# Performance work log

Measured on AMD Instinct MI355X. Metric: run time of the kernel, lower is better.

Reference implementation:

```python
import jax, jax.numpy as jnp
import numpy as np

NUM_HEADS = 16


def setup_inputs() -> dict:
    key = jax.random.key(0)
    ks = jax.random.split(key, 6)
    B, S, D = 2, 2048, 1024
    hidden_states = jax.random.normal(ks[0], (B, S, D), dtype=jnp.float32)
    attention_mask = jnp.zeros((B, 1, 1, S), dtype=jnp.float32)  # additive mask
    # Linear weights stored as [in, out] (equivalent to torch weight.T)
    W_qkv = jax.random.normal(ks[1], (D, 3 * D), dtype=jnp.float32) * (1.0 / np.sqrt(D))
    b_qkv = jnp.zeros((3 * D,), dtype=jnp.float32)
    W_proj = jax.random.normal(ks[2], (D, D), dtype=jnp.float32) * (1.0 / np.sqrt(D))
    b_proj = jnp.zeros((D,), dtype=jnp.float32)
    return {
        "hidden_states": hidden_states,
        "attention_mask": attention_mask,
        "W_qkv": W_qkv,
        "b_qkv": b_qkv,
        "W_proj": W_proj,
        "b_proj": b_proj,
    }


def reference(hidden_states, attention_mask, W_qkv, b_qkv, W_proj, b_proj):
    B, S, D = hidden_states.shape
    H = NUM_HEADS
    hd = D // H
    scale = 1.0 / jnp.sqrt(jnp.asarray(hd, hidden_states.dtype))

    qkv = hidden_states @ W_qkv + b_qkv            # [B,S,3D]
    q, k, v = jnp.split(qkv, 3, axis=-1)
    # [B,S,D] -> [B,H,S,hd]
    split_heads = lambda t: t.reshape(B, S, H, hd).transpose(0, 2, 1, 3)
    q, k, v = split_heads(q), split_heads(k), split_heads(v)

    scores = jnp.einsum("bhqd,bhkd->bhqk", q, k) * scale + attention_mask
    attn = jax.nn.softmax(scores, axis=-1)
    ctx = jnp.einsum("bhqk,bhkd->bhqd", attn, v)   # [B,H,S,hd]
    ctx = ctx.transpose(0, 2, 1, 3).reshape(B, S, D)
    return ctx @ W_proj + b_proj
```

## Files before the change

kernel.cpp:

```cpp
#include <hip/hip_runtime.h>
#include <hip/hip_bf16.h>

typedef short short8 __attribute__((ext_vector_type(8)));
typedef float floatx4 __attribute__((ext_vector_type(4)));

#define S_LEN 2048
#define DMODEL 1024
#define NH 16
#define HD 64
#define BATCH 2

static __device__ __forceinline__ short f2bf(float x) {
    __hip_bfloat16 h = __float2bfloat16(x);
    return *(short*)&h;
}

static __device__ __forceinline__ void async_ld16(const __hip_bfloat16* g, __hip_bfloat16* l) {
    __builtin_amdgcn_global_load_lds(
        (const __attribute__((address_space(1))) unsigned int*)g,
        (__attribute__((address_space(3))) unsigned int*)l, 16, 0, 0);
}

__global__ __launch_bounds__(256) void cvt_kernel(const float* __restrict__ X,
                                                  __hip_bfloat16* __restrict__ Y) {
    int i = (blockIdx.x * 256 + threadIdx.x) * 8;
    floatx4 f0 = *(const floatx4*)&X[i];
    floatx4 f1 = *(const floatx4*)&X[i + 4];
    short8 s;
    s[0] = f2bf(f0[0]); s[1] = f2bf(f0[1]); s[2] = f2bf(f0[2]); s[3] = f2bf(f0[3]);
    s[4] = f2bf(f1[0]); s[5] = f2bf(f1[1]); s[6] = f2bf(f1[2]); s[7] = f2bf(f1[3]);
    *(short8*)&Y[i] = s;
}

__global__ void transpose_kernel(const float* __restrict__ W,
                                 __hip_bfloat16* __restrict__ Wt, int K, int N) {
    __shared__ float tile[32][33];
    int n0 = blockIdx.x * 32, k0 = blockIdx.y * 32;
    int tx = threadIdx.x, ty = threadIdx.y;
#pragma unroll
    for (int i = 0; i < 32; i += 8)
        tile[ty + i][tx] = W[(size_t)(k0 + ty + i) * N + n0 + tx];
    __syncthreads();
#pragma unroll
    for (int i = 0; i < 32; i += 8)
        Wt[(size_t)(n0 + ty + i) * K + k0 + tx] = __float2bfloat16(tile[tx][ty + i]);
}

__global__ __launch_bounds__(256) void gemm128(
    const __hip_bfloat16* __restrict__ A, const __hip_bfloat16* __restrict__ Bt,
    const float* __restrict__ bias, float* __restrict__ Cf,
    __hip_bfloat16* __restrict__ Qp, __hip_bfloat16* __restrict__ Kp,
    __hip_bfloat16* __restrict__ Vt, int M, int N, int K, int mode) {
    __shared__ __align__(16) __hip_bfloat16 As[128 * 32];
    __shared__ __align__(16) __hip_bfloat16 Bs[128 * 32];
    const int m0 = blockIdx.y * 128, n0 = blockIdx.x * 128;
    const int t = threadIdx.x;
    const int wave = t >> 6, lane = t & 63;
    const int quad = lane >> 4, m16 = lane & 15;
    const int wm = (wave >> 1) * 64, wn = (wave & 1) * 64;
    const int srow = lane >> 2, scol = (lane & 3) * 8;

    floatx4 acc[4][4] = {};
    for (int k0 = 0; k0 < K; k0 += 32) {
#pragma unroll
        for (int i = 0; i < 2; i++) {
            const int rbase = wave * 32 + i * 16;
            async_ld16(&A[(size_t)(m0 + rbase + srow) * K + k0 + scol], &As[rbase * 32]);
            async_ld16(&Bt[(size_t)(n0 + rbase + srow) * K + k0 + scol], &Bs[rbase * 32]);
        }
        __syncthreads();
        short8 af[4], bfr[4];
#pragma unroll
        for (int i = 0; i < 4; i++)
            af[i] = *(const short8*)&As[(wm + i * 16 + m16) * 32 + quad * 8];
#pragma unroll
        for (int j = 0; j < 4; j++)
            bfr[j] = *(const short8*)&Bs[(wn + j * 16 + m16) * 32 + quad * 8];
#pragma unroll
        for (int i = 0; i < 4; i++)
#pragma unroll
            for (int j = 0; j < 4; j++)
                acc[i][j] = __builtin_amdgcn_mfma_f32_16x16x32_bf16(af[i], bfr[j], acc[i][j], 0, 0, 0);
        __syncthreads();
    }
#pragma unroll
    for (int i = 0; i < 4; i++)
#pragma unroll
        for (int j = 0; j < 4; j++) {
            int col = n0 + wn + j * 16 + m16;
            float bv = bias[col];
#pragma unroll
            for (int r = 0; r < 4; r++) {
                int row = m0 + wm + i * 16 + quad * 4 + r;
                float v = acc[i][j][r] + bv;
                if (mode == 0) {
                    Cf[(size_t)row * N + col] = v;
                } else {
                    __hip_bfloat16 hv = __float2bfloat16(v);
                    int tt = col >> 10, rem = col & 1023;
                    int h = rem >> 6, d = rem & 63;
                    int b = row >> 11, s = row & 2047;
                    if (tt == 0)      Qp[((size_t)(b * NH + h) * S_LEN + s) * HD + d] = hv;
                    else if (tt == 1) Kp[((size_t)(b * NH + h) * S_LEN + s) * HD + d] = hv;
                    else              Vt[((size_t)(b * NH + h) * HD + d) * S_LEN + s] = hv;
                }
            }
        }
}

__global__ __launch_bounds__(256) void attn_kernel(
    const __hip_bfloat16* __restrict__ Q,
    const __hip_bfloat16* __restrict__ K,
    const __hip_bfloat16* __restrict__ Vt,
    const float* __restrict__ mask,
    __hip_bfloat16* __restrict__ ctx) {
    __shared__ __align__(16) __hip_bfloat16 Ks[2][32 * 64];
    __shared__ __align__(16) __hip_bfloat16 Vs[2][64 * 32];
    __shared__ __align__(16) __hip_bfloat16 Ps[4][16][40];
    const int bh = blockIdx.x;
    const int b = bh >> 4, h = bh & 15;
    const int t = threadIdx.x, wave = t >> 6, lane = t & 63;
    const int quad = lane >> 4, m16 = lane & 15;
    const int qbase = blockIdx.y * 64 + wave * 16;
    const __hip_bfloat16* Qh = Q + (size_t)bh * S_LEN * HD;
    const __hip_bfloat16* Kh = K + (size_t)bh * S_LEN * HD;
    const __hip_bfloat16* Vh = Vt + (size_t)bh * HD * S_LEN;
    const float* mb = mask + (size_t)b * S_LEN;
    const float LOG2E = 1.44269504f;
    const float scale2 = 0.125f * LOG2E;
    const float M_FIX2 = 20.0f * LOG2E;

    const int kr = lane >> 3, kc = lane & 7;
    const size_t kgoff = (size_t)(wave * 8 + kr) * HD + ((kc ^ (kr & 7)) * 8);
    const int vr = lane >> 2, vc = lane & 3;
    const size_t vgoff = (size_t)(wave * 16 + vr) * S_LEN + ((vc ^ (vr & 3)) * 8);
    __hip_bfloat16* kdst0 = &Ks[0][wave * 512]; __hip_bfloat16* kdst1 = &Ks[1][wave * 512];
    __hip_bfloat16* vdst0 = &Vs[0][wave * 512]; __hip_bfloat16* vdst1 = &Vs[1][wave * 512];

    short8 aq0 = *(const short8*)&Qh[(size_t)(qbase + m16) * HD + quad * 8];
    short8 aq1 = *(const short8*)&Qh[(size_t)(qbase + m16) * HD + 32 + quad * 8];

    const short ONEB = (short)0x3F80;
    const short8 ones = {ONEB, ONEB, ONEB, ONEB, ONEB, ONEB, ONEB, ONEB};

    async_ld16(&Kh[kgoff], kdst0);
    async_ld16(&Vh[vgoff], vdst0);
    __syncthreads();

    floatx4 o[4] = {};
    floatx4 lacc = {};

    const int swk = m16 & 7;
    const int pc0 = (((m16 >> 3) ^ quad) << 3) | (m16 & 7);
    const int pc1 = ((((m16 >> 3) + 2) ^ quad) << 3) | (m16 & 7);
    const int apoff = (quad ^ ((m16 >> 2) & 3)) * 8;

    for (int it = 0; it < S_LEN / 32; it++) {
        const int k0 = it * 32;
        const int cur = it & 1;
        if (it < S_LEN / 32 - 1) {
            async_ld16(&Kh[(size_t)(k0 + 32) * HD + kgoff], cur ? kdst0 : kdst1);
            async_ld16(&Vh[(size_t)(k0 + 32) + vgoff], cur ? vdst0 : vdst1);
        }

        const __hip_bfloat16* Kc = Ks[cur];
        short8 bk00 = *(const short8*)&Kc[m16 * 64 + ((quad ^ swk) * 8)];
        short8 bk01 = *(const short8*)&Kc[m16 * 64 + (((quad + 4) ^ swk) * 8)];
        short8 bk10 = *(const short8*)&Kc[(16 + m16) * 64 + ((quad ^ swk) * 8)];
        short8 bk11 = *(const short8*)&Kc[(16 + m16) * 64 + (((quad + 4) ^ swk) * 8)];
        floatx4 sc0 = {}, sc1 = {};
        __builtin_amdgcn_s_setprio(1);
        sc0 = __builtin_amdgcn_mfma_f32_16x16x32_bf16(aq0, bk00, sc0, 0, 0, 0);
        sc0 = __builtin_amdgcn_mfma_f32_16x16x32_bf16(aq1, bk01, sc0, 0, 0, 0);
        sc1 = __builtin_amdgcn_mfma_f32_16x16x32_bf16(aq0, bk10, sc1, 0, 0, 0);
        sc1 = __builtin_amdgcn_mfma_f32_16x16x32_bf16(aq1, bk11, sc1, 0, 0, 0);
        __builtin_amdgcn_s_setprio(0);

        float mk0 = mb[k0 + m16] * LOG2E - M_FIX2;
        float mk1 = mb[k0 + 16 + m16] * LOG2E - M_FIX2;
#pragma unroll
        for (int r = 0; r < 4; r++) {
            float p0 = __builtin_amdgcn_exp2f(sc0[r] * scale2 + mk0);
            float p1 = __builtin_amdgcn_exp2f(sc1[r] * scale2 + mk1);
            Ps[wave][quad * 4 + r][pc0] = __float2bfloat16(p0);
            Ps[wave][quad * 4 + r][pc1] = __float2bfloat16(p1);
        }
        short8 ap = *(const short8*)&Ps[wave][m16][apoff];
        const __hip_bfloat16* Vc = Vs[cur];
        __builtin_amdgcn_s_setprio(1);
        lacc = __builtin_amdgcn_mfma_f32_16x16x32_bf16(ap, ones, lacc, 0, 0, 0);
#pragma unroll
        for (int tt = 0; tt < 4; tt++) {
            const int d = tt * 16 + m16;
            short8 bv = *(const short8*)&Vc[d * 32 + ((quad ^ (d & 3)) * 8)];
            o[tt] = __builtin_amdgcn_mfma_f32_16x16x32_bf16(ap, bv, o[tt], 0, 0, 0);
        }
        __builtin_amdgcn_s_setprio(0);
        __syncthreads();
    }

    float li[4];
#pragma unroll
    for (int r = 0; r < 4; r++) li[r] = 1.0f / lacc[r];
#pragma unroll
    for (int tt = 0; tt < 4; tt++)
#pragma unroll
        for (int r = 0; r < 4; r++) {
            int srow = qbase + quad * 4 + r;
            int d = tt * 16 + m16;
            float v = o[tt][r] * li[r];
            ctx[((size_t)b * S_LEN + srow) * DMODEL + h * HD + d] = __float2bfloat16(v);
        }
}

extern "C" void kernel_launch(void* const* d_in, const int* in_sizes, int n_in,
                              void* d_out, int out_size, void* d_ws, size_t ws_size,
                              hipStream_t stream) {
    (void)in_sizes; (void)n_in; (void)out_size; (void)ws_size;
    const float* hidden = (const float*)d_in[0];
    const float* mask   = (const float*)d_in[1];
    const float* Wqkv   = (const float*)d_in[2];
    const float* bqkv   = (const float*)d_in[3];
    const float* Wproj  = (const float*)d_in[4];
    const float* bproj  = (const float*)d_in[5];
    float* out = (float*)d_out;

    __hip_bfloat16* ws = (__hip_bfloat16*)d_ws;
    const size_t Q4 = 4u * 1024 * 1024;
    __hip_bfloat16* Qp      = ws;
    __hip_bfloat16* Kp      = ws + 1 * Q4;
    __hip_bfloat16* Vt      = ws + 2 * Q4;
    __hip_bfloat16* hid_bf  = ws + 3 * Q4;
    __hip_bfloat16* ctx     = ws + 3 * Q4;
    __hip_bfloat16* Wqkv_t  = ws + 4 * Q4;
    __hip_bfloat16* Wproj_t = ws + 4 * Q4;

    cvt_kernel<<<dim3(4 * 1024 * 1024 / 2048), 256, 0, stream>>>(hidden, hid_bf);
    transpose_kernel<<<dim3(3072 / 32, 1024 / 32), dim3(32, 8), 0, stream>>>(Wqkv, Wqkv_t, 1024, 3072);

    gemm128<<<dim3(3072 / 128, 4096 / 128), 256, 0, stream>>>(
        hid_bf, Wqkv_t, bqkv, nullptr, Qp, Kp, Vt, BATCH * S_LEN, 3 * DMODEL, DMODEL, 1);

    transpose_kernel<<<dim3(1024 / 32, 1024 / 32), dim3(32, 8), 0, stream>>>(Wproj, Wproj_t, 1024, 1024);

    attn_kernel<<<dim3(BATCH * NH, S_LEN / 64), 256, 0, stream>>>(Qp, Kp, Vt, mask, ctx);

    gemm128<<<dim3(1024 / 128, 4096 / 128), 256, 0, stream>>>(
        ctx, Wproj_t, bproj, out, nullptr, nullptr, nullptr, BATCH * S_LEN, DMODEL, DMODEL, 0);
}
```

Baseline: 228.5 us.

## Keep attention probabilities in registers via transposed QK^T and lane swizzle

The attention kernel now computes S^T (K as the A operand, Q as B), so each lane holds the probabilities it needs for the PV MFMA. A ds_swizzle exchange between lane pairs replaces the per-wave LDS round-trip through the Ps buffer. The key/value tile grows from 32 to 64 keys per iteration, which halves the loop trip count and barriers and doubles LDS for K/V, and launch_bounds now requests 4 blocks per CU. The lane mapping is intricate, so a permutation error would silently give wrong results, and the larger tiles raise register and LDS pressure.

```diff
diff --git a/kernel.cpp b/kernel.cpp
--- a/kernel.cpp
+++ b/kernel.cpp
@@ -3,6 +3,7 @@
 
 typedef short short8 __attribute__((ext_vector_type(8)));
 typedef float floatx4 __attribute__((ext_vector_type(4)));
+typedef int intx4 __attribute__((ext_vector_type(4)));
 
 #define S_LEN 2048
 #define DMODEL 1024
@@ -13,6 +14,12 @@
 static __device__ __forceinline__ short f2bf(float x) {
     __hip_bfloat16 h = __float2bfloat16(x);
     return *(short*)&h;
+}
+
+static __device__ __forceinline__ unsigned pk2(float lo, float hi) {
+    unsigned a = (unsigned)(unsigned short)f2bf(lo);
+    unsigned b = (unsigned)(unsigned short)f2bf(hi);
+    return a | (b << 16);
 }
 
 static __device__ __forceinline__ void async_ld16(const __hip_bfloat16* g, __hip_bfloat16* l) {
@@ -108,15 +115,14 @@
         }
 }
 
-__global__ __launch_bounds__(256) void attn_kernel(
+__global__ __launch_bounds__(256, 4) void attn_kernel(
     const __hip_bfloat16* __restrict__ Q,
     const __hip_bfloat16* __restrict__ K,
     const __hip_bfloat16* __restrict__ Vt,
     const float* __restrict__ mask,
     __hip_bfloat16* __restrict__ ctx) {
-    __shared__ __align__(16) __hip_bfloat16 Ks[2][32 * 64];
-    __shared__ __align__(16) __hip_bfloat16 Vs[2][64 * 32];
-    __shared__ __align__(16) __hip_bfloat16 Ps[4][16][40];
+    __shared__ __align__(16) __hip_bfloat16 Ks[2][64 * 64];
+    __shared__ __align__(16) __hip_bfloat16 Vs[2][64 * 64];
     const int bh = blockIdx.x;
     const int b = bh >> 4, h = bh & 15;
     const int t = threadIdx.x, wave = t >> 6, lane = t & 63;
@@ -130,12 +136,11 @@
     const float scale2 = 0.125f * LOG2E;
     const float M_FIX2 = 20.0f * LOG2E;
 
-    const int kr = lane >> 3, kc = lane & 7;
-    const size_t kgoff = (size_t)(wave * 8 + kr) * HD + ((kc ^ (kr & 7)) * 8);
-    const int vr = lane >> 2, vc = lane & 3;
-    const size_t vgoff = (size_t)(wave * 16 + vr) * S_LEN + ((vc ^ (vr & 3)) * 8);
-    __hip_bfloat16* kdst0 = &Ks[0][wave * 512]; __hip_bfloat16* kdst1 = &Ks[1][wave * 512];
-    __hip_bfloat16* vdst0 = &Vs[0][wave * 512]; __hip_bfloat16* vdst1 = &Vs[1][wave * 512];
+    const int r8 = lane >> 3, c8 = lane & 7;
+    const int kg0 = (wave * 16 + r8) * HD + ((c8 ^ r8) * 8);
+    const int kg1 = (wave * 16 + 8 + r8) * HD + ((c8 ^ r8) * 8);
+    const int vg0 = (wave * 16 + r8) * S_LEN + ((c8 ^ r8) * 8);
+    const int vg1 = (wave * 16 + 8 + r8) * S_LEN + ((c8 ^ r8) * 8);
 
     short8 aq0 = *(const short8*)&Qh[(size_t)(qbase + m16) * HD + quad * 8];
     short8 aq1 = *(const short8*)&Qh[(size_t)(qbase + m16) * HD + 32 + quad * 8];
@@ -143,57 +148,97 @@
     const short ONEB = (short)0x3F80;
     const short8 ones = {ONEB, ONEB, ONEB, ONEB, ONEB, ONEB, ONEB, ONEB};
 
-    async_ld16(&Kh[kgoff], kdst0);
-    async_ld16(&Vh[vgoff], vdst0);
+    {
+        __hip_bfloat16* kd = &Ks[0][wave * 16 * 64];
+        async_ld16(&Kh[kg0], kd);
+        async_ld16(&Kh[kg1], kd + 512);
+        __hip_bfloat16* vd = &Vs[0][wave * 16 * 64];
+        async_ld16(&Vh[vg0], vd);
+        async_ld16(&Vh[vg1], vd + 512);
+    }
     __syncthreads();
 
     floatx4 o[4] = {};
     floatx4 lacc = {};
-
     const int swk = m16 & 7;
-    const int pc0 = (((m16 >> 3) ^ quad) << 3) | (m16 & 7);
-    const int pc1 = ((((m16 >> 3) + 2) ^ quad) << 3) | (m16 & 7);
-    const int apoff = (quad ^ ((m16 >> 2) & 3)) * 8;
-
-    for (int it = 0; it < S_LEN / 32; it++) {
-        const int k0 = it * 32;
+    const int e = quad & 1;
+    const int cA = ((quad & 1) << 2) | (quad >> 1);
+    const int cB = cA | 2;
+    const int vsA = (cA ^ swk) * 8;
+    const int vsB = (cB ^ swk) * 8;
+
+    for (int it = 0; it < S_LEN / 64; it++) {
+        const int k0 = it * 64;
         const int cur = it & 1;
-        if (it < S_LEN / 32 - 1) {
-            async_ld16(&Kh[(size_t)(k0 + 32) * HD + kgoff], cur ? kdst0 : kdst1);
-            async_ld16(&Vh[(size_t)(k0 + 32) + vgoff], cur ? vdst0 : vdst1);
+        if (it < S_LEN / 64 - 1) {
+            __hip_bfloat16* kd = &Ks[cur ^ 1][wave * 16 * 64];
+            async_ld16(&Kh[(k0 + 64) * HD + kg0], kd);
+            async_ld16(&Kh[(k0 + 64) * HD + kg1], kd + 512);
+            __hip_bfloat16* vd = &Vs[cur ^ 1][wave * 16 * 64];
+            async_ld16(&Vh[(k0 + 64) + vg0], vd);
+            async_ld16(&Vh[(k0 + 64) + vg1], vd + 512);
         }
 
         const __hip_bfloat16* Kc = Ks[cur];
-        short8 bk00 = *(const short8*)&Kc[m16 * 64 + ((quad ^ swk) * 8)];
-        short8 bk01 = *(const short8*)&Kc[m16 * 64 + (((quad + 4) ^ swk) * 8)];
-        short8 bk10 = *(const short8*)&Kc[(16 + m16) * 64 + ((quad ^ swk) * 8)];
-        short8 bk11 = *(const short8*)&Kc[(16 + m16) * 64 + (((quad + 4) ^ swk) * 8)];
-        floatx4 sc0 = {}, sc1 = {};
+        floatx4 sc[4] = {};
         __builtin_amdgcn_s_setprio(1);
-        sc0 = __builtin_amdgcn_mfma_f32_16x16x32_bf16(aq0, bk00, sc0, 0, 0, 0);
-        sc0 = __builtin_amdgcn_mfma_f32_16x16x32_bf16(aq1, bk01, sc0, 0, 0, 0);
-        sc1 = __builtin_amdgcn_mfma_f32_16x16x32_bf16(aq0, bk10, sc1, 0, 0, 0);
-        sc1 = __builtin_amdgcn_mfma_f32_16x16x32_bf16(aq1, bk11, sc1, 0, 0, 0);
+#pragma unroll
+        for (int kt = 0; kt < 4; kt++) {
+            const int row = kt * 16 + m16;
+            short8 ak0 = *(const short8*)&Kc[row * 64 + ((quad ^ swk) * 8)];
+            short8 ak1 = *(const short8*)&Kc[row * 64 + (((quad + 4) ^ swk) * 8)];
+            sc[kt] = __builtin_amdgcn_mfma_f32_16x16x32_bf16(ak0, aq0, sc[kt], 0, 0, 0);
+            sc[kt] = __builtin_amdgcn_mfma_f32_16x16x32_bf16(ak1, aq1, sc[kt], 0, 0, 0);
+        }
         __builtin_amdgcn_s_setprio(0);
 
-        float mk0 = mb[k0 + m16] * LOG2E - M_FIX2;
-        float mk1 = mb[k0 + 16 + m16] * LOG2E - M_FIX2;
-#pragma unroll
-        for (int r = 0; r < 4; r++) {
-            float p0 = __builtin_amdgcn_exp2f(sc0[r] * scale2 + mk0);
-            float p1 = __builtin_amdgcn_exp2f(sc1[r] * scale2 + mk1);
-            Ps[wave][quad * 4 + r][pc0] = __float2bfloat16(p0);
-            Ps[wave][quad * 4 + r][pc1] = __float2bfloat16(p1);
-        }
-        short8 ap = *(const short8*)&Ps[wave][m16][apoff];
+        unsigned dk[4][2];
+#pragma unroll
+        for (int kt = 0; kt < 4; kt++) {
+            floatx4 mv = *(const floatx4*)&mb[k0 + kt * 16 + quad * 4];
+            float p0 = __builtin_amdgcn_exp2f(
+                __builtin_fmaf(sc[kt][0], scale2, __builtin_fmaf(mv[0], LOG2E, -M_FIX2)));
+            float p1 = __builtin_amdgcn_exp2f(
+                __builtin_fmaf(sc[kt][1], scale2, __builtin_fmaf(mv[1], LOG2E, -M_FIX2)));
+            float p2 = __builtin_amdgcn_exp2f(
+                __builtin_fmaf(sc[kt][2], scale2, __builtin_fmaf(mv[2], LOG2E, -M_FIX2)));
+            float p3 = __builtin_amdgcn_exp2f(
+                __builtin_fmaf(sc[kt][3], scale2, __builtin_fmaf(mv[3], LOG2E, -M_FIX2)));
+            dk[kt][0] = pk2(p0, p1);
+            dk[kt][1] = pk2(p2, p3);
+        }
+
+        unsigned t0 = e ? dk[0][0] : dk[2][0];
+        unsigned t1 = e ? dk[0][1] : dk[2][1];
+        unsigned t2 = e ? dk[1][0] : dk[3][0];
+        unsigned t3 = e ? dk[1][1] : dk[3][1];
+        unsigned r0 = (unsigned)__builtin_amdgcn_ds_swizzle((int)t0, 0x401F);
+        unsigned r1 = (unsigned)__builtin_amdgcn_ds_swizzle((int)t1, 0x401F);
+        unsigned r2 = (unsigned)__builtin_amdgcn_ds_swizzle((int)t2, 0x401F);
+        unsigned r3 = (unsigned)__builtin_amdgcn_ds_swizzle((int)t3, 0x401F);
+        intx4 wa, wb;
+        wa[0] = (int)(e ? r0 : dk[0][0]);
+        wa[1] = (int)(e ? r1 : dk[0][1]);
+        wa[2] = (int)(e ? dk[2][0] : r0);
+        wa[3] = (int)(e ? dk[2][1] : r1);
+        wb[0] = (int)(e ? r2 : dk[1][0]);
+        wb[1] = (int)(e ? r3 : dk[1][1]);
+        wb[2] = (int)(e ? dk[3][0] : r2);
+        wb[3] = (int)(e ? dk[3][1] : r3);
+        short8 apA = *(short8*)&wa;
+        short8 apB = *(short8*)&wb;
+
         const __hip_bfloat16* Vc = Vs[cur];
         __builtin_amdgcn_s_setprio(1);
-        lacc = __builtin_amdgcn_mfma_f32_16x16x32_bf16(ap, ones, lacc, 0, 0, 0);
+        lacc = __builtin_amdgcn_mfma_f32_16x16x32_bf16(apA, ones, lacc, 0, 0, 0);
+        lacc = __builtin_amdgcn_mfma_f32_16x16x32_bf16(apB, ones, lacc, 0, 0, 0);
 #pragma unroll
         for (int tt = 0; tt < 4; tt++) {
             const int d = tt * 16 + m16;
-            short8 bv = *(const short8*)&Vc[d * 32 + ((quad ^ (d & 3)) * 8)];
-            o[tt] = __builtin_amdgcn_mfma_f32_16x16x32_bf16(ap, bv, o[tt], 0, 0, 0);
+            short8 bvA = *(const short8*)&Vc[d * 64 + vsA];
+            short8 bvB = *(const short8*)&Vc[d * 64 + vsB];
+            o[tt] = __builtin_amdgcn_mfma_f32_16x16x32_bf16(apA, bvA, o[tt], 0, 0, 0);
+            o[tt] = __builtin_amdgcn_mfma_f32_16x16x32_bf16(apB, bvB, o[tt], 0, 0, 0);
         }
         __builtin_amdgcn_s_setprio(0);
         __syncthreads();
```

After: 219.4 us. -4.0%, faster.
